# Optimization experiments

Hardware: AMD Instinct MI355X
Metric: run time of the kernel (lower is better)

## Reference

```python
import jax, jax.numpy as jnp
import numpy as np

D_MODEL = 512

def setup_inputs() -> dict:
    key = jax.random.key(0)
    k1, k2, k3, k4, k5 = jax.random.split(key, 5)
    x = jax.random.normal(k1, (8, D_MODEL, 2048), dtype=jnp.float32)
    s = 1.0 / np.sqrt(D_MODEL)
    W_qkv = jax.random.uniform(k2, (D_MODEL, 3 * D_MODEL), dtype=jnp.float32, minval=-s, maxval=s)
    b_qkv = jax.random.uniform(k3, (3 * D_MODEL,), dtype=jnp.float32, minval=-s, maxval=s)
    W_proj = jax.random.uniform(k4, (D_MODEL, D_MODEL), dtype=jnp.float32, minval=-s, maxval=s)
    b_proj = jax.random.uniform(k5, (D_MODEL,), dtype=jnp.float32, minval=-s, maxval=s)
    return {"x": x, "W_qkv": W_qkv, "b_qkv": b_qkv, "W_proj": W_proj, "b_proj": b_proj}

def reference(x, W_qkv, b_qkv, W_proj, b_proj):
    # x: [B, L, N] with L == d_model; attend across the N variable axis
    xt = jnp.swapaxes(x, 1, 2)                      # [B, N, L]
    L = xt.shape[-1]
    qkv = xt @ W_qkv + b_qkv                        # [B, N, 3L]
    q, k, v = jnp.split(qkv, 3, axis=-1)            # each [B, N, L]
    attn = jnp.einsum('bnd,bmd->bnm', q, k) / jnp.sqrt(jnp.float32(L))
    attn = jax.nn.softmax(attn, axis=-1)            # [B, N, N]
    out = jnp.einsum('bnm,bmd->bnd', attn, v)       # [B, N, L]
    out = out @ W_proj + b_proj                     # [B, N, L]
    return jnp.swapaxes(out, 1, 2)                  # [B, L, N]
```

## Files before the change

### kernel.cpp

```cpp
#include <hip/hip_runtime.h>

#define NVAR 2048
#define DM   512
#define J3   1536

typedef _Float16 f16;
typedef _Float16 f16x8 __attribute__((ext_vector_type(8)));
typedef _Float16 f16x4 __attribute__((ext_vector_type(4)));
typedef float    f32x4 __attribute__((ext_vector_type(4)));

#define SBAR() do { asm volatile("s_barrier" ::: "memory"); \
                    __builtin_amdgcn_sched_barrier(0); } while(0)
#define WAITVM0() do { asm volatile("s_waitcnt vmcnt(0)" ::: "memory"); \
                       __builtin_amdgcn_sched_barrier(0); } while(0)

__global__ __launch_bounds__(256)
void k_tr(const float* __restrict__ src, f16* __restrict__ dst,
          int R, int C, long bsSrc, long bsDst) {
    __shared__ float t[64][65];
    const float* s = src + (size_t)blockIdx.z * bsSrc;
    f16* d = dst + (size_t)blockIdx.z * bsDst;
    const int c0 = blockIdx.x * 64, r0 = blockIdx.y * 64;
    const int tx = threadIdx.x & 63, w = threadIdx.x >> 6;
#pragma unroll
    for (int i = 0; i < 16; ++i) {
        int r = w * 16 + i;
        t[r][tx] = s[(size_t)(r0 + r) * C + c0 + tx];
    }
    __syncthreads();
#pragma unroll
    for (int i = 0; i < 16; ++i) {
        int c = w * 16 + i;
        d[(size_t)(c0 + c) * R + r0 + tx] = (f16)t[tx][c];
    }
}

template<int MODE>
__global__ __launch_bounds__(256)
void gemm_f16(const f16* __restrict__ A, const f16* __restrict__ B,
              long bsA, long bsB, int lda, int ldb, int K, int nbx,
              const float* __restrict__ bias, float scale,
              f16* __restrict__ o0, f16* __restrict__ o1, f16* __restrict__ o2,
              float* __restrict__ of) {
    __shared__ f16 sA[2][128 * 64];
    __shared__ f16 sB[2][128 * 64];
    const int tid  = threadIdx.x;
    const int lane = tid & 63;
    const int w    = __builtin_amdgcn_readfirstlane(tid >> 6);
    const int wm   = (w >> 1) * 64;
    const int wn   = (w & 1) * 64;
    const int z    = blockIdx.x;
    const int bid  = blockIdx.y;
    const int bxA  = bid % nbx;
    const int bxB  = bid / nbx;

    const f16* Ab = A + (size_t)z * bsA + (size_t)bxA * 128 * lda;
    const f16* Bb = B + (size_t)z * bsB + (size_t)bxB * 128 * ldb;

    int srcA[4], srcB[4];
#pragma unroll
    for (int i = 0; i < 4; ++i) {
        int slot = i * 256 + tid;
        int row  = slot >> 3;
        int s    = (slot & 7) ^ (row & 7);
        srcA[i] = row * lda + s * 8;
        srcB[i] = row * ldb + s * 8;
    }

    auto STAGE = [&](int kt) {
        f16* dA = sA[kt & 1];
        f16* dB = sB[kt & 1];
        const int k0 = kt * 64;
#pragma unroll
        for (int i = 0; i < 4; ++i)
            __builtin_amdgcn_global_load_lds(
                (const __attribute__((address_space(1))) void*)(Ab + srcA[i] + k0),
                (__attribute__((address_space(3))) void*)(dA + i * 2048 + w * 512),
                16, 0, 0);
#pragma unroll
        for (int i = 0; i < 4; ++i)
            __builtin_amdgcn_global_load_lds(
                (const __attribute__((address_space(1))) void*)(Bb + srcB[i] + k0),
                (__attribute__((address_space(3))) void*)(sB[kt & 1] + i * 2048 + w * 512),
                16, 0, 0);
        (void)dB;
    };

    f32x4 acc[4][4] = {};
    float rs[4] = {};
    const int NT = K >> 6;

    STAGE(0);
    WAITVM0();
    SBAR();

    for (int t = 0; t < NT; ++t) {
        const f16* pA = sA[t & 1];
        const f16* pB = sB[t & 1];
        if (t + 1 < NT) STAGE(t + 1);
        __builtin_amdgcn_s_setprio(1);
#pragma unroll
        for (int kh = 0; kh < 2; ++kh) {
            f16x8 av[4], bv[4];
#pragma unroll
            for (int mi = 0; mi < 4; ++mi) {
                int r = wm + mi * 16 + (lane & 15);
                int s = (kh * 4 + (lane >> 4)) ^ (r & 7);
                av[mi] = *(const f16x8*)(pA + r * 64 + s * 8);
            }
#pragma unroll
            for (int nj = 0; nj < 4; ++nj) {
                int r = wn + nj * 16 + (lane & 15);
                int s = (kh * 4 + (lane >> 4)) ^ (r & 7);
                bv[nj] = *(const f16x8*)(pB + r * 64 + s * 8);
            }
            if constexpr (MODE == 2) {
#pragma unroll
                for (int nj = 0; nj < 4; ++nj)
#pragma unroll
                    for (int e = 0; e < 8; ++e)
                        rs[nj] += (float)bv[nj][e];
            }
#pragma unroll
            for (int mi = 0; mi < 4; ++mi)
#pragma unroll
                for (int nj = 0; nj < 4; ++nj)
                    acc[mi][nj] = __builtin_amdgcn_mfma_f32_16x16x32_f16(
                        av[mi], bv[nj], acc[mi][nj], 0, 0, 0);
        }
        __builtin_amdgcn_s_setprio(0);
        if (t + 1 < NT) {
            WAITVM0();
            SBAR();
        }
    }

    const int rb0 = bxA * 128 + wm + (lane >> 4) * 4;
    const int cb0 = bxB * 128 + wn + (lane & 15);

    if (MODE == 0) {
        const int seg = (bxA * 128) >> 9;
#pragma unroll
        for (int mi = 0; mi < 4; ++mi) {
            const int j = rb0 + mi * 16;
            const f32x4 b4 = *(const f32x4*)(bias + j);
#pragma unroll
            for (int nj = 0; nj < 4; ++nj) {
                const int n = cb0 + nj * 16;
                if (seg == 2) {
#pragma unroll
                    for (int r = 0; r < 4; ++r)
                        o2[((size_t)z * DM + (j - 1024 + r)) * NVAR + n] =
                            (f16)(acc[mi][nj][r] + b4[r]);
                } else {
                    f16* dst = seg ? o1 : o0;
                    const int jj = seg ? j - 512 : j;
                    f16x4 vv;
#pragma unroll
                    for (int r = 0; r < 4; ++r) vv[r] = (f16)(acc[mi][nj][r] + b4[r]);
                    *(f16x4*)(dst + ((size_t)z * NVAR + n) * DM + jj) = vv;
                }
            }
        }
    } else if (MODE == 1) {
#pragma unroll
        for (int mi = 0; mi < 4; ++mi)
#pragma unroll
            for (int nj = 0; nj < 4; ++nj) {
                f16x4 vv;
#pragma unroll
                for (int r = 0; r < 4; ++r)
                    vv[r] = (f16)__expf(acc[mi][nj][r] * scale);
                *(f16x4*)(o0 + ((size_t)z * NVAR + cb0 + nj * 16) * NVAR
                               + rb0 + mi * 16) = vv;
            }
    } else if (MODE == 2) {
#pragma unroll
        for (int nj = 0; nj < 4; ++nj) {
            rs[nj] += __shfl_xor(rs[nj], 16);
            rs[nj] += __shfl_xor(rs[nj], 32);
            rs[nj] = 1.0f / rs[nj];
        }
#pragma unroll
        for (int mi = 0; mi < 4; ++mi)
#pragma unroll
            for (int nj = 0; nj < 4; ++nj) {
                f16x4 vv;
#pragma unroll
                for (int r = 0; r < 4; ++r)
                    vv[r] = (f16)(acc[mi][nj][r] * rs[nj]);
                *(f16x4*)(o0 + ((size_t)z * NVAR + cb0 + nj * 16) * DM
                               + rb0 + mi * 16) = vv;
            }
    } else {
#pragma unroll
        for (int mi = 0; mi < 4; ++mi)
#pragma unroll
            for (int nj = 0; nj < 4; ++nj) {
                const int l = cb0 + nj * 16;
                const float bb = bias[l];
                f32x4 vv;
#pragma unroll
                for (int r = 0; r < 4; ++r) vv[r] = acc[mi][nj][r] + bb;
                *(f32x4*)(of + ((size_t)z * DM + l) * NVAR + rb0 + mi * 16) = vv;
            }
    }
}

extern "C" void kernel_launch(void* const* d_in, const int* in_sizes, int n_in,
                              void* d_out, int out_size, void* d_ws, size_t ws_size,
                              hipStream_t stream) {
    const float* x     = (const float*)d_in[0];
    const float* Wqkv  = (const float*)d_in[1];
    const float* bqkv  = (const float*)d_in[2];
    const float* Wproj = (const float*)d_in[3];
    const float* bproj = (const float*)d_in[4];
    float* out = (float*)d_out;

    const size_t PB = (size_t)NVAR * DM;
    f16* xT  = (f16*)d_ws;
    f16* q   = xT + 8 * PB;
    f16* kk  = q  + 8 * PB;
    f16* vT  = kk + 8 * PB;
    f16* S   = vT + 8 * PB;
    f16* O   = S  + (size_t)8 * NVAR * NVAR;
    f16* WqT = O  + 8 * PB;
    f16* WpT = WqT + (size_t)J3 * DM;

    k_tr<<<dim3(NVAR / 64, DM / 64, 8), 256, 0, stream>>>(
        x, xT, DM, NVAR, (long)DM * NVAR, (long)NVAR * DM);
    k_tr<<<dim3(J3 / 64, DM / 64, 1), 256, 0, stream>>>(Wqkv, WqT, DM, J3, 0, 0);
    k_tr<<<dim3(DM / 64, DM / 64, 1), 256, 0, stream>>>(Wproj, WpT, DM, DM, 0, 0);

    gemm_f16<0><<<dim3(8, 12 * 16), 256, 0, stream>>>(
        WqT, xT, 0, (long)NVAR * DM, DM, DM, DM, 12,
        bqkv, 1.f, q, kk, vT, nullptr);

    gemm_f16<1><<<dim3(8, 16 * 16), 256, 0, stream>>>(
        kk, q, (long)NVAR * DM, (long)NVAR * DM, DM, DM, DM, 16,
        nullptr, 0.044194173824159216f, S, nullptr, nullptr, nullptr);

    gemm_f16<2><<<dim3(8, 4 * 16), 256, 0, stream>>>(
        vT, S, (long)DM * NVAR, (long)NVAR * NVAR, NVAR, NVAR, NVAR, 4,
        nullptr, 1.f, O, nullptr, nullptr, nullptr);

    gemm_f16<3><<<dim3(8, 16 * 4), 256, 0, stream>>>(
        O, WpT, (long)NVAR * DM, 0, DM, DM, DM, 16,
        bproj, 1.f, nullptr, nullptr, nullptr, out);
}
```

Before: 192.5 us.

## Use 256x128 tiles with 8 waves and triple-buffered split-stage GEMM pipeline

Enlarges the GEMM block tile to 256x128 with 512 threads (8 waves). Replaces double buffering with a three-deep LDS ring, prefetching two k-tiles ahead. Each k-step is split into two half-phases that interleave global-to-LDS staging with the MFMA work, using partial vmcnt waits. The aim is to hide global load latency and raise operand reuse per block. The cost is more LDS per block (about 144KB), which limits occupancy, and fewer blocks in the grid.

```diff
diff --git a/kernel.cpp b/kernel.cpp
--- a/kernel.cpp
+++ b/kernel.cpp
@@ -11,8 +11,13 @@
 
 #define SBAR() do { asm volatile("s_barrier" ::: "memory"); \
                     __builtin_amdgcn_sched_barrier(0); } while(0)
-#define WAITVM0() do { asm volatile("s_waitcnt vmcnt(0)" ::: "memory"); \
+#define WAITVM(n) do { asm volatile("s_waitcnt vmcnt(" #n ")" ::: "memory"); \
                        __builtin_amdgcn_sched_barrier(0); } while(0)
+#define WAITLGKM0() do { asm volatile("s_waitcnt lgkmcnt(0)" ::: "memory"); \
+                         __builtin_amdgcn_sched_barrier(0); } while(0)
+#define GLOAD(gp, lp) __builtin_amdgcn_global_load_lds( \
+    (const __attribute__((address_space(1))) void*)(gp), \
+    (__attribute__((address_space(3))) void*)(lp), 16, 0, 0)
 
 __global__ __launch_bounds__(256)
 void k_tr(const float* __restrict__ src, f16* __restrict__ dst,
@@ -36,14 +41,16 @@
 }
 
 template<int MODE>
-__global__ __launch_bounds__(256)
+__global__ __launch_bounds__(512)
 void gemm_f16(const f16* __restrict__ A, const f16* __restrict__ B,
               long bsA, long bsB, int lda, int ldb, int K, int nbx,
               const float* __restrict__ bias, float scale,
               f16* __restrict__ o0, f16* __restrict__ o1, f16* __restrict__ o2,
               float* __restrict__ of) {
-    __shared__ f16 sA[2][128 * 64];
-    __shared__ f16 sB[2][128 * 64];
+    constexpr int ASZ = 256 * 64;
+    constexpr int BSZ = 128 * 64;
+    __shared__ f16 sA[3 * ASZ];
+    __shared__ f16 sB[3 * BSZ];
     const int tid  = threadIdx.x;
     const int lane = tid & 63;
     const int w    = __builtin_amdgcn_readfirstlane(tid >> 6);
@@ -54,92 +61,124 @@
     const int bxA  = bid % nbx;
     const int bxB  = bid / nbx;
 
-    const f16* Ab = A + (size_t)z * bsA + (size_t)bxA * 128 * lda;
+    const f16* Ab = A + (size_t)z * bsA + (size_t)bxA * 256 * lda;
     const f16* Bb = B + (size_t)z * bsB + (size_t)bxB * 128 * ldb;
 
-    int srcA[4], srcB[4];
+    int srcA[4], srcB[2];
 #pragma unroll
     for (int i = 0; i < 4; ++i) {
-        int slot = i * 256 + tid;
-        int row  = slot >> 3;
-        int s    = (slot & 7) ^ (row & 7);
+        int slot = i * 512 + tid, row = slot >> 3, s = (slot & 7) ^ (row & 7);
         srcA[i] = row * lda + s * 8;
+    }
+#pragma unroll
+    for (int i = 0; i < 2; ++i) {
+        int slot = i * 512 + tid, row = slot >> 3, s = (slot & 7) ^ (row & 7);
         srcB[i] = row * ldb + s * 8;
     }
 
-    auto STAGE = [&](int kt) {
-        f16* dA = sA[kt & 1];
-        f16* dB = sB[kt & 1];
+    auto STG1 = [&](int kt) {
+        f16* dA = sA + (kt % 3) * ASZ;
         const int k0 = kt * 64;
 #pragma unroll
-        for (int i = 0; i < 4; ++i)
-            __builtin_amdgcn_global_load_lds(
-                (const __attribute__((address_space(1))) void*)(Ab + srcA[i] + k0),
-                (__attribute__((address_space(3))) void*)(dA + i * 2048 + w * 512),
-                16, 0, 0);
-#pragma unroll
-        for (int i = 0; i < 4; ++i)
-            __builtin_amdgcn_global_load_lds(
-                (const __attribute__((address_space(1))) void*)(Bb + srcB[i] + k0),
-                (__attribute__((address_space(3))) void*)(sB[kt & 1] + i * 2048 + w * 512),
-                16, 0, 0);
-        (void)dB;
+        for (int i = 0; i < 3; ++i)
+            GLOAD(Ab + srcA[i] + k0, dA + i * 4096 + w * 512);
     };
+    auto STG2 = [&](int kt) {
+        f16* dA = sA + (kt % 3) * ASZ;
+        f16* dB = sB + (kt % 3) * BSZ;
+        const int k0 = kt * 64;
+        GLOAD(Ab + srcA[3] + k0, dA + 3 * 4096 + w * 512);
+#pragma unroll
+        for (int i = 0; i < 2; ++i)
+            GLOAD(Bb + srcB[i] + k0, dB + i * 4096 + w * 512);
+    };
+
+    int koff[2];
+#pragma unroll
+    for (int ks = 0; ks < 2; ++ks)
+        koff[ks] = (((ks * 4 + (lane >> 4)) ^ (lane & 7))) * 8;
+    const int rowA = (wm + (lane & 15)) * 64;
+    const int rowB = (wn + (lane & 15)) * 64;
 
     f32x4 acc[4][4] = {};
     float rs[4] = {};
     const int NT = K >> 6;
 
-    STAGE(0);
-    WAITVM0();
+    STG1(0); STG2(0);
+    STG1(1); STG2(1);
+    WAITVM(6);
     SBAR();
 
     for (int t = 0; t < NT; ++t) {
-        const f16* pA = sA[t & 1];
-        const f16* pB = sB[t & 1];
-        if (t + 1 < NT) STAGE(t + 1);
+        const f16* pA = sA + (t % 3) * ASZ;
+        const f16* pB = sB + (t % 3) * BSZ;
+        const bool stg = (t + 2 < NT);
+
+        f16x8 bv[4][2], av[2][2];
+#pragma unroll
+        for (int nj = 0; nj < 4; ++nj)
+#pragma unroll
+            for (int ks = 0; ks < 2; ++ks)
+                bv[nj][ks] = *(const f16x8*)(pB + rowB + nj * 1024 + koff[ks]);
+#pragma unroll
+        for (int mi = 0; mi < 2; ++mi)
+#pragma unroll
+            for (int ks = 0; ks < 2; ++ks)
+                av[mi][ks] = *(const f16x8*)(pA + rowA + mi * 1024 + koff[ks]);
+        if (stg) STG1(t + 2);
+        SBAR();
+        WAITLGKM0();
         __builtin_amdgcn_s_setprio(1);
-#pragma unroll
-        for (int kh = 0; kh < 2; ++kh) {
-            f16x8 av[4], bv[4];
-#pragma unroll
-            for (int mi = 0; mi < 4; ++mi) {
-                int r = wm + mi * 16 + (lane & 15);
-                int s = (kh * 4 + (lane >> 4)) ^ (r & 7);
-                av[mi] = *(const f16x8*)(pA + r * 64 + s * 8);
-            }
-#pragma unroll
-            for (int nj = 0; nj < 4; ++nj) {
-                int r = wn + nj * 16 + (lane & 15);
-                int s = (kh * 4 + (lane >> 4)) ^ (r & 7);
-                bv[nj] = *(const f16x8*)(pB + r * 64 + s * 8);
-            }
-            if constexpr (MODE == 2) {
-#pragma unroll
-                for (int nj = 0; nj < 4; ++nj)
+        if constexpr (MODE == 2) {
+#pragma unroll
+            for (int nj = 0; nj < 4; ++nj)
+#pragma unroll
+                for (int ks = 0; ks < 2; ++ks)
 #pragma unroll
                     for (int e = 0; e < 8; ++e)
-                        rs[nj] += (float)bv[nj][e];
-            }
-#pragma unroll
-            for (int mi = 0; mi < 4; ++mi)
-#pragma unroll
-                for (int nj = 0; nj < 4; ++nj)
+                        rs[nj] += (float)bv[nj][ks][e];
+        }
+#pragma unroll
+        for (int mi = 0; mi < 2; ++mi)
+#pragma unroll
+            for (int nj = 0; nj < 4; ++nj)
+#pragma unroll
+                for (int ks = 0; ks < 2; ++ks)
                     acc[mi][nj] = __builtin_amdgcn_mfma_f32_16x16x32_f16(
-                        av[mi], bv[nj], acc[mi][nj], 0, 0, 0);
-        }
+                        av[mi][ks], bv[nj][ks], acc[mi][nj], 0, 0, 0);
+        __builtin_amdgcn_s_setprio(0);
+        SBAR();
+
+#pragma unroll
+        for (int mi = 0; mi < 2; ++mi)
+#pragma unroll
+            for (int ks = 0; ks < 2; ++ks)
+                av[mi][ks] = *(const f16x8*)(pA + rowA + (2 + mi) * 1024 + koff[ks]);
+        if (stg) STG2(t + 2);
+        SBAR();
+        WAITLGKM0();
+        __builtin_amdgcn_s_setprio(1);
+#pragma unroll
+        for (int mi = 0; mi < 2; ++mi)
+#pragma unroll
+            for (int nj = 0; nj < 4; ++nj)
+#pragma unroll
+                for (int ks = 0; ks < 2; ++ks)
+                    acc[2 + mi][nj] = __builtin_amdgcn_mfma_f32_16x16x32_f16(
+                        av[mi][ks], bv[nj][ks], acc[2 + mi][nj], 0, 0, 0);
         __builtin_amdgcn_s_setprio(0);
         if (t + 1 < NT) {
-            WAITVM0();
+            if (stg) { WAITVM(6); }
+            else     { WAITVM(0); }
             SBAR();
         }
     }
 
-    const int rb0 = bxA * 128 + wm + (lane >> 4) * 4;
+    const int rb0 = bxA * 256 + wm + (lane >> 4) * 4;
     const int cb0 = bxB * 128 + wn + (lane & 15);
 
     if (MODE == 0) {
-        const int seg = (bxA * 128) >> 9;
+        const int seg = (bxA * 256) >> 9;
 #pragma unroll
         for (int mi = 0; mi < 4; ++mi) {
             const int j = rb0 + mi * 16;
@@ -232,19 +271,19 @@
     k_tr<<<dim3(J3 / 64, DM / 64, 1), 256, 0, stream>>>(Wqkv, WqT, DM, J3, 0, 0);
     k_tr<<<dim3(DM / 64, DM / 64, 1), 256, 0, stream>>>(Wproj, WpT, DM, DM, 0, 0);
 
-    gemm_f16<0><<<dim3(8, 12 * 16), 256, 0, stream>>>(
-        WqT, xT, 0, (long)NVAR * DM, DM, DM, DM, 12,
+    gemm_f16<0><<<dim3(8, 6 * 16), 512, 0, stream>>>(
+        WqT, xT, 0, (long)NVAR * DM, DM, DM, DM, 6,
         bqkv, 1.f, q, kk, vT, nullptr);
 
-    gemm_f16<1><<<dim3(8, 16 * 16), 256, 0, stream>>>(
-        kk, q, (long)NVAR * DM, (long)NVAR * DM, DM, DM, DM, 16,
+    gemm_f16<1><<<dim3(8, 8 * 16), 512, 0, stream>>>(
+        kk, q, (long)NVAR * DM, (long)NVAR * DM, DM, DM, DM, 8,
         nullptr, 0.044194173824159216f, S, nullptr, nullptr, nullptr);
 
-    gemm_f16<2><<<dim3(8, 4 * 16), 256, 0, stream>>>(
-        vT, S, (long)DM * NVAR, (long)NVAR * NVAR, NVAR, NVAR, NVAR, 4,
+    gemm_f16<2><<<dim3(8, 2 * 16), 512, 0, stream>>>(
+        vT, S, (long)DM * NVAR, (long)NVAR * NVAR, NVAR, NVAR, NVAR, 2,
         nullptr, 1.f, O, nullptr, nullptr, nullptr);
 
-    gemm_f16<3><<<dim3(8, 16 * 4), 256, 0, stream>>>(
-        O, WpT, (long)NVAR * DM, 0, DM, DM, DM, 16,
+    gemm_f16<3><<<dim3(8, 8 * 4), 512, 0, stream>>>(
+        O, WpT, (long)NVAR * DM, 0, DM, DM, DM, 8,
         bproj, 1.f, nullptr, nullptr, nullptr, out);
 }
```

New measurement: 192.4 us. About the same (-0.1%).
